# Kernel optimization log

Measured on AMD Instinct MI355X. Metric: run time of the kernel, lower is better.

The kernel has to match this reference:

```python
import jax, jax.numpy as jnp
import numpy as np

B, S, D, H = 64, 256, 1024, 1024
F0, F1 = 1024, 1024
STDV = 1.0 / np.sqrt(H)


def setup_inputs() -> dict:
    key = jax.random.key(0)
    ks = jax.random.split(key, 14)
    u = lambda k, shape: jax.random.uniform(k, shape, jnp.float32, -STDV, STDV)
    return {
        "input_feats": jax.random.normal(ks[0], (B, S, D), jnp.float32),
        "feat0": jax.random.normal(ks[1], (B, S, F0), jnp.float32),
        "feat1": jax.random.normal(ks[2], (B, S, F1), jnp.float32),
        "weight_ih": u(ks[3], (3 * H, D)),
        "weight_hh": u(ks[4], (3 * H, H)),
        "weight_fh0": u(ks[5], (2 * H, F0)),
        "weight_fh1": u(ks[6], (2 * H, F1)),
        "bias_ih": u(ks[7], (3 * H,)),
        "bias_hh": u(ks[8], (3 * H,)),
        "bias_fh0": u(ks[9], (2 * H,)),
        "bias_fh1": u(ks[10], (2 * H,)),
    }


def reference(input_feats, feat0, feat1, weight_ih, weight_hh, weight_fh0,
              weight_fh1, bias_ih, bias_hh, bias_fh0, bias_fh1):
    hid = weight_hh.shape[1]
    # Input-to-gate and feature-to-gate projections have no recurrence:
    # batch them over all timesteps up front (same math as per-step F.linear).
    gi = input_feats @ weight_ih.T + bias_ih                      # [B,S,3H]
    gf = (feat0 @ weight_fh0.T + feat1 @ weight_fh1.T
          + bias_fh0 + bias_fh1)                                  # [B,S,2H]
    gi_t = jnp.swapaxes(gi, 0, 1)                                 # [S,B,3H]
    gf_t = jnp.swapaxes(gf, 0, 1)                                 # [S,B,2H]

    def step(hx, xs):
        gi_s, gf_s = xs
        gh = hx @ weight_hh.T + bias_hh                           # [B,3H]
        i_r, i_i, i_n = jnp.split(gi_s, 3, axis=1)
        h_r, h_i, h_n = jnp.split(gh, 3, axis=1)
        f_r, f_i = jnp.split(gf_s, 2, axis=1)
        resetgate = jax.nn.sigmoid(i_r + h_r + f_r)
        inputgate = jax.nn.sigmoid(i_i + h_i + f_i)
        newgate = jnp.tanh(i_n + resetgate * h_n)
        hy = newgate + inputgate * (hx - newgate)
        return hy, hy

    h0 = jnp.zeros((input_feats.shape[0], hid), input_feats.dtype)
    h_last, ys = jax.lax.scan(step, h0, (gi_t, gf_t))
    output = jnp.swapaxes(ys, 0, 1)                               # [B,S,H]
    return output, h_last
```

## Files before the change

### kernel.cpp

```cpp
#include <hip/hip_runtime.h>

typedef unsigned short u16;
typedef __attribute__((ext_vector_type(8))) short short8;
typedef __attribute__((ext_vector_type(4))) float f32x4;
typedef __attribute__((ext_vector_type(4))) unsigned u32x4;

#define BB 64
#define SS 256
#define HH 1024
#define NG 3072
#define KK 1024
#define NOUT ((size_t)BB * SS * HH)

#define OFF_GSUM 0ull
#define OFF_HB0 100663296ull
#define OFF_HB1 100794368ull
#define OFF_BAR 100925440ull
#define WS_NEED 100925952ull

__device__ __forceinline__ float bf2f_u(unsigned x) {
  unsigned u = x << 16;
  float f;
  __builtin_memcpy(&f, &u, 4);
  return f;
}
__device__ __forceinline__ u16 f2bf(float f) {
  unsigned u;
  __builtin_memcpy(&u, &f, 4);
  u = (u + 0x7fffu + ((u >> 16) & 1u)) >> 16;
  return (u16)u;
}
__device__ __forceinline__ short8 cvt8(f32x4 lo, f32x4 hi) {
  union { unsigned u[4]; short8 s; } r;
  asm("v_cvt_pk_bf16_f32 %0, %1, %2" : "=v"(r.u[0]) : "v"(lo[0]), "v"(lo[1]));
  asm("v_cvt_pk_bf16_f32 %0, %1, %2" : "=v"(r.u[1]) : "v"(lo[2]), "v"(lo[3]));
  asm("v_cvt_pk_bf16_f32 %0, %1, %2" : "=v"(r.u[2]) : "v"(hi[0]), "v"(hi[1]));
  asm("v_cvt_pk_bf16_f32 %0, %1, %2" : "=v"(r.u[3]) : "v"(hi[2]), "v"(hi[3]));
  return r.s;
}
__device__ __forceinline__ float sigmoidf_(float x) {
  return __builtin_amdgcn_rcpf(1.f + __expf(-x));
}
__device__ __forceinline__ float tanhf_(float x) {
  return 2.f * __builtin_amdgcn_rcpf(1.f + __expf(-2.f * x)) - 1.f;
}

typedef const __attribute__((address_space(1))) void* gcptr;
typedef __attribute__((address_space(3))) void* lptr;

__global__ __launch_bounds__(256) void gemm_fused(
    const float* __restrict__ X, const float* __restrict__ F0, const float* __restrict__ F1,
    const float* __restrict__ Wih, const float* __restrict__ Wf0, const float* __restrict__ Wf1,
    const float* __restrict__ bih, const float* __restrict__ bf0, const float* __restrict__ bf1,
    u16* __restrict__ C) {
  __shared__ __align__(16) float ldsA[128 * 32];
  __shared__ __align__(16) float ldsB[128 * 32];
  const int t = threadIdx.x;
  const int nwg = gridDim.x;
  const int cpx = nwg >> 3;
  const int wg = (blockIdx.x & 7) * cpx + (blockIdx.x >> 3);
  const int ntn = NG / 128;
  const int m0 = (wg / ntn) * 128;
  const int n0 = (wg % ntn) * 128;
  const int lane = t & 63, wv = t >> 6;
  const int wm = wv >> 1, wn = wv & 1;

  f32x4 acc[4][4] = {};

  const int nsrc = (n0 < 2048) ? 3 : 1;
  for (int src = 0; src < nsrc; ++src) {
    const float* Ap = (src == 0) ? X : ((src == 1) ? F0 : F1);
    const float* Wp = (src == 0) ? Wih : ((src == 1) ? Wf0 : Wf1);
    const float* Abase = Ap + (size_t)m0 * KK;
    const float* Wbase = Wp + (size_t)n0 * KK;
    for (int k0 = 0; k0 < KK; k0 += 32) {
#pragma unroll
      for (int c = 0; c < 4; ++c) {
        const int idx = c * 256 + t;
        const int row = idx >> 3, q = idx & 7;
        const int qs = q ^ (row & 7);
        __builtin_amdgcn_global_load_lds((gcptr)(Abase + (size_t)row * KK + k0 + qs * 4),
                                         (lptr)(&ldsA[idx * 4]), 16, 0, 0);
        __builtin_amdgcn_global_load_lds((gcptr)(Wbase + (size_t)row * KK + k0 + qs * 4),
                                         (lptr)(&ldsB[idx * 4]), 16, 0, 0);
      }
      __syncthreads();
      short8 af[4], bw[4];
      const int g0 = (lane >> 4) * 2;
#pragma unroll
      for (int i = 0; i < 4; ++i) {
        {
          const int row = wm * 64 + i * 16 + (lane & 15);
          const int ga = g0 ^ (row & 7), gb = (g0 + 1) ^ (row & 7);
          f32x4 lo = *(const f32x4*)&ldsA[row * 32 + ga * 4];
          f32x4 hi = *(const f32x4*)&ldsA[row * 32 + gb * 4];
          af[i] = cvt8(lo, hi);
        }
        {
          const int row = wn * 64 + i * 16 + (lane & 15);
          const int ga = g0 ^ (row & 7), gb = (g0 + 1) ^ (row & 7);
          f32x4 lo = *(const f32x4*)&ldsB[row * 32 + ga * 4];
          f32x4 hi = *(const f32x4*)&ldsB[row * 32 + gb * 4];
          bw[i] = cvt8(lo, hi);
        }
      }
#pragma unroll
      for (int i = 0; i < 4; ++i)
#pragma unroll
        for (int j = 0; j < 4; ++j)
          acc[i][j] = __builtin_amdgcn_mfma_f32_16x16x32_bf16(af[i], bw[j], acc[i][j], 0, 0, 0);
      __syncthreads();
    }
  }
#pragma unroll
  for (int j = 0; j < 4; ++j) {
    const int col = n0 + wn * 64 + j * 16 + (lane & 15);
    float bias = bih[col];
    if (col < 2048) bias += bf0[col] + bf1[col];
#pragma unroll
    for (int i = 0; i < 4; ++i) {
      const int row = m0 + wm * 64 + i * 16 + (lane >> 4) * 4;
#pragma unroll
      for (int r = 0; r < 4; ++r)
        C[(size_t)(row + r) * NG + col] = f2bf(acc[i][j][r] + bias);
    }
  }
}

#define SB0() __builtin_amdgcn_sched_barrier(0)

#define ISSUE8(buf, bkk)                                                        \
  _Pragma("unroll")                                                             \
  for (int i_ = 0; i_ < 8; ++i_)                                                \
    asm volatile("global_load_dwordx4 %0, %1, off sc0 sc1"                      \
                 : "=&v"(buf[i_]) : "v"(ap + ((bkk) + i_) * 32));

#define CONSUME8(buf, bkk)                                                      \
  _Pragma("unroll")                                                             \
  for (int i_ = 0; i_ < 8; ++i_) {                                              \
    const int ko_ = ((bkk) + i_) * 64 + kb;                                     \
    short8 br_ = *(const short8*)(s0 + (ko_ ^ sw));                             \
    short8 bj_ = *(const short8*)(s1 + (ko_ ^ sw));                             \
    short8 bn_ = *(const short8*)(s2 + (ko_ ^ sw));                             \
    ar = __builtin_amdgcn_mfma_f32_16x16x32_bf16(buf[i_], br_, ar, 0, 0, 0);    \
    ai = __builtin_amdgcn_mfma_f32_16x16x32_bf16(buf[i_], bj_, ai, 0, 0, 0);    \
    an = __builtin_amdgcn_mfma_f32_16x16x32_bf16(buf[i_], bn_, an, 0, 0, 0);    \
  }

#define ISSUE_GSUM(snext)                                                       \
  _Pragma("unroll")                                                             \
  for (int r_ = 0; r_ < 4; ++r_) {                                              \
    const u16* gp_ = gsum + ((size_t)(mb + quad * 4 + r_) * 256 + (size_t)(snext)) * 3072 + jl; \
    asm volatile("global_load_ushort %0, %1, off" : "=&v"(pgu[r_ * 3 + 0]) : "v"(gp_));          \
    asm volatile("global_load_ushort %0, %1, off" : "=&v"(pgu[r_ * 3 + 1]) : "v"(gp_ + 1024));   \
    asm volatile("global_load_ushort %0, %1, off" : "=&v"(pgu[r_ * 3 + 2]) : "v"(gp_ + 2048));   \
  }

__global__ __launch_bounds__(256, 1) void scan_kernel(
    const u16* __restrict__ gsum, const float* __restrict__ Whh, const float* __restrict__ bhh,
    u16* __restrict__ h0buf, u16* __restrict__ h1buf,
    float* __restrict__ out, unsigned* __restrict__ bar) {
  extern __shared__ u16 wlds[];
  const int t = threadIdx.x, w = blockIdx.x;
  const int j0 = w * 16;
  for (int c = t; c < 48 * 128; c += 256) {
    int q = c >> 7, chunk = c & 127;
    int g = q >> 4, i = q & 15;
    const float* wf = Whh + ((size_t)(g * 1024 + j0 + i)) * 1024 + chunk * 8;
    short8 v = cvt8(*(const f32x4*)wf, *(const f32x4*)(wf + 4));
    *(short8*)((char*)wlds + q * 2048 + ((chunk * 16) ^ (i << 4))) = v;
  }
  const int lane = t & 63;
  const int bi = lane & 15;
  const int quad = lane >> 4;
  const int jl = j0 + bi;
  const int mb = (t >> 6) * 16;
  const float bhr = bhh[jl];
  const float bhi = bhh[1024 + jl];
  const float bhn = bhh[2048 + jl];
  __syncthreads();

  float hreg[4] = {0.f, 0.f, 0.f, 0.f};

  const int kb = quad * 16;
  const int sw = bi << 4;
  const char* wbytes = (const char*)wlds;
  const char* s0 = wbytes + (size_t)(0 + bi) * 2048;
  const char* s1 = wbytes + (size_t)(16 + bi) * 2048;
  const char* s2 = wbytes + (size_t)(32 + bi) * 2048;

  unsigned* myctr = bar + (w & 7);

  unsigned pgu[12];
  ISSUE_GSUM(0);
  asm volatile("s_waitcnt vmcnt(0)" ::: "memory");
  SB0();

  short8 aA[8], aB[8], aC[8], aD[8];
  for (int s = 0; s < 256; ++s) {
    f32x4 ar = {0.f, 0.f, 0.f, 0.f};
    f32x4 ai = {0.f, 0.f, 0.f, 0.f};
    f32x4 an = {0.f, 0.f, 0.f, 0.f};
    if (s > 0) {
      asm volatile("s_waitcnt vmcnt(24)" ::: "memory");
      SB0();
      CONSUME8(aA, 0);
      asm volatile("s_waitcnt vmcnt(16)" ::: "memory");
      SB0();
      CONSUME8(aB, 8);
      asm volatile("s_waitcnt vmcnt(8)" ::: "memory");
      SB0();
      CONSUME8(aC, 16);
      asm volatile("s_waitcnt vmcnt(0)" ::: "memory");
      SB0();
      CONSUME8(aD, 24);
      SB0();
    }
    u16* hw = (s & 1) ? h0buf : h1buf;
    float hy4[4];
    unsigned hv4[4];
#pragma unroll
    for (int r = 0; r < 4; ++r) {
      float rg = sigmoidf_(bf2f_u(pgu[r * 3 + 0]) + ar[r] + bhr);
      float ig = sigmoidf_(bf2f_u(pgu[r * 3 + 1]) + ai[r] + bhi);
      float ng = tanhf_(bf2f_u(pgu[r * 3 + 2]) + rg * (an[r] + bhn));
      float hy = ng + ig * (hreg[r] - ng);
      hreg[r] = hy;
      hy4[r] = hy;
      hv4[r] = (unsigned)f2bf(hy);
    }
    if (s < 255) {
#pragma unroll
      for (int r = 0; r < 4; ++r) {
        int b = mb + quad * 4 + r;
        asm volatile("global_store_short %0, %1, off sc0 sc1"
                     :: "v"(hw + (size_t)b * 1024 + jl), "v"(hv4[r]) : "memory");
      }
    }
#pragma unroll
    for (int r = 0; r < 4; ++r) {
      int b = mb + quad * 4 + r;
      size_t m = (size_t)b * 256 + s;
      asm volatile("global_store_dword %0, %1, off nt"
                   :: "v"(out + m * 1024 + jl), "v"(hy4[r]) : "memory");
    }
    if (s < 255) {
      ISSUE_GSUM(s + 1);
      asm volatile("s_waitcnt vmcnt(16)" ::: "memory");
      SB0();
      __builtin_amdgcn_s_barrier();
      if (t == 0) {
        unsigned one = 1;
        asm volatile("global_atomic_add %0, %1, off" :: "v"(myctr), "v"(one) : "memory");
      }
      if (lane == 0) {
        const unsigned target = 64u * (unsigned)(s + 1);
        for (;;) {
          u32x4 va, vb;
          asm volatile("global_load_dwordx4 %0, %2, off sc0 sc1\n\t"
                       "global_load_dwordx4 %1, %2, off offset:16 sc0 sc1\n\t"
                       "s_waitcnt vmcnt(0)"
                       : "=&v"(va), "=&v"(vb) : "v"(bar) : "memory");
          unsigned sum = va[0] + va[1] + va[2] + va[3] + vb[0] + vb[1] + vb[2] + vb[3];
          if (sum >= target) break;
          __builtin_amdgcn_s_sleep(1);
        }
      }
      SB0();
      const u16* ap = hw + (size_t)(mb + bi) * 1024 + quad * 8;
      ISSUE8(aA, 0);
      ISSUE8(aB, 8);
      ISSUE8(aC, 16);
      ISSUE8(aD, 24);
      SB0();
    }
  }
#pragma unroll
  for (int r = 0; r < 4; ++r) {
    int b = mb + quad * 4 + r;
    out[NOUT + (size_t)b * 1024 + jl] = hreg[r];
  }
}

extern "C" void kernel_launch(void* const* d_in, const int* in_sizes, int n_in,
                              void* d_out, int out_size, void* d_ws, size_t ws_size,
                              hipStream_t stream) {
  if (ws_size < WS_NEED) return;
  const float* x   = (const float*)d_in[0];
  const float* f0  = (const float*)d_in[1];
  const float* f1  = (const float*)d_in[2];
  const float* wih = (const float*)d_in[3];
  const float* whh = (const float*)d_in[4];
  const float* wf0 = (const float*)d_in[5];
  const float* wf1 = (const float*)d_in[6];
  const float* bih = (const float*)d_in[7];
  const float* bhh = (const float*)d_in[8];
  const float* bf0 = (const float*)d_in[9];
  const float* bf1 = (const float*)d_in[10];

  char* ws = (char*)d_ws;
  u16* gsum = (u16*)(ws + OFF_GSUM);
  u16* hb0 = (u16*)(ws + OFF_HB0);
  u16* hb1 = (u16*)(ws + OFF_HB1);
  unsigned* bar = (unsigned*)(ws + OFF_BAR);

  hipMemsetAsync(bar, 0, 128, stream);
  hipMemsetAsync(hb0, 0, 131072, stream);
  hipMemsetAsync(hb1, 0, 131072, stream);

  gemm_fused<<<dim3(3072), dim3(256), 0, stream>>>(x, f0, f1, wih, wf0, wf1, bih, bf0, bf1, gsum);

  hipFuncSetAttribute(reinterpret_cast<const void*>(&scan_kernel),
                      hipFuncAttributeMaxDynamicSharedMemorySize, 98304);
  scan_kernel<<<dim3(64), dim3(256), 98304, stream>>>(gsum, whh, bhh, hb0, hb1, (float*)d_out, bar);
}
```

Baseline: 2.613 ms.

## Add dedicated sync wavefront with staged per-quarter barrier relay through LDS

Adds a fifth wavefront per block that performs the grid-wide atomic arrive and polls the counters, publishing progress through an LDS relay variable. Counters are regrouped so each covers a contiguous group of 8 blocks, which lets the compute waves start loading each quarter of the hidden state as soon as the blocks producing it have arrived instead of waiting for all blocks. The goal is to overlap the cross-block barrier with the loads of h for the next step. The cost is an extra wave and LDS polling spins, plus timeout guards that could let a wave read stale data if a block is very late.

Result: slower. 4.458 ms (+70.6%).

```diff
diff --git a/kernel.cpp b/kernel.cpp
--- a/kernel.cpp
+++ b/kernel.cpp
@@ -156,14 +156,22 @@
     asm volatile("global_load_ushort %0, %1, off" : "=&v"(pgu[r_ * 3 + 2]) : "v"(gp_ + 2048));   \
   }
 
-__global__ __launch_bounds__(256, 1) void scan_kernel(
+#define POLL(K)                                                                 \
+  if (lane == 0) {                                                              \
+    int guard_ = 0;                                                             \
+    while (*(volatile int*)&relay < 4 * s + (K) + 1 && ++guard_ < (1 << 22)) {} \
+  }                                                                             \
+  SB0();
+
+__global__ __launch_bounds__(320, 1) void scan_kernel(
     const u16* __restrict__ gsum, const float* __restrict__ Whh, const float* __restrict__ bhh,
     u16* __restrict__ h0buf, u16* __restrict__ h1buf,
     float* __restrict__ out, unsigned* __restrict__ bar) {
   extern __shared__ u16 wlds[];
+  __shared__ int relay;
   const int t = threadIdx.x, w = blockIdx.x;
   const int j0 = w * 16;
-  for (int c = t; c < 48 * 128; c += 256) {
+  for (int c = t; c < 48 * 128; c += 320) {
     int q = c >> 7, chunk = c & 127;
     int g = q >> 4, i = q & 15;
     const float* wf = Whh + ((size_t)(g * 1024 + j0 + i)) * 1024 + chunk * 8;
@@ -171,16 +179,17 @@
     *(short8*)((char*)wlds + q * 2048 + ((chunk * 16) ^ (i << 4))) = v;
   }
   const int lane = t & 63;
+  const int wv = t >> 6;
   const int bi = lane & 15;
   const int quad = lane >> 4;
   const int jl = j0 + bi;
-  const int mb = (t >> 6) * 16;
+  const int mb = (wv & 3) * 16;
   const float bhr = bhh[jl];
   const float bhi = bhh[1024 + jl];
   const float bhn = bhh[2048 + jl];
+  unsigned* myctr = bar + (w >> 3);
+  if (t == 0) relay = 0;
   __syncthreads();
-
-  float hreg[4] = {0.f, 0.f, 0.f, 0.f};
 
   const int kb = quad * 16;
   const int sw = bi << 4;
@@ -189,8 +198,34 @@
   const char* s1 = wbytes + (size_t)(16 + bi) * 2048;
   const char* s2 = wbytes + (size_t)(32 + bi) * 2048;
 
-  unsigned* myctr = bar + (w & 7);
-
+  if (wv == 4) {
+    for (int s = 0; s < 255; ++s) {
+      __builtin_amdgcn_s_barrier();
+      if (lane == 0) {
+        unsigned one = 1;
+        asm volatile("global_atomic_add %0, %1, off" :: "v"(myctr), "v"(one) : "memory");
+        const unsigned tgt = 16u * (unsigned)(s + 1);
+        int lvl = 0, guard = 0;
+        while (lvl < 4) {
+          u32x4 va, vb;
+          asm volatile("global_load_dwordx4 %0, %2, off sc0 sc1\n\t"
+                       "global_load_dwordx4 %1, %2, off offset:16 sc0 sc1\n\t"
+                       "s_waitcnt vmcnt(0)"
+                       : "=&v"(va), "=&v"(vb) : "v"(bar) : "memory");
+          unsigned p0 = va[0] + va[1], p1 = va[2] + va[3];
+          unsigned p2 = vb[0] + vb[1], p3 = vb[2] + vb[3];
+          int nl = 0;
+          if (p0 >= tgt) { nl = 1; if (p1 >= tgt) { nl = 2; if (p2 >= tgt) { nl = 3; if (p3 >= tgt) nl = 4; } } }
+          if (nl > lvl) { lvl = nl; *(volatile int*)&relay = 4 * s + lvl; }
+          if (++guard > (1 << 18)) { *(volatile int*)&relay = 4 * s + 4; break; }
+          if (lvl < 4) __builtin_amdgcn_s_sleep(1);
+        }
+      }
+    }
+    return;
+  }
+
+  float hreg[4] = {0.f, 0.f, 0.f, 0.f};
   unsigned pgu[12];
   ISSUE_GSUM(0);
   asm volatile("s_waitcnt vmcnt(0)" ::: "memory");
@@ -249,28 +284,14 @@
       asm volatile("s_waitcnt vmcnt(16)" ::: "memory");
       SB0();
       __builtin_amdgcn_s_barrier();
-      if (t == 0) {
-        unsigned one = 1;
-        asm volatile("global_atomic_add %0, %1, off" :: "v"(myctr), "v"(one) : "memory");
-      }
-      if (lane == 0) {
-        const unsigned target = 64u * (unsigned)(s + 1);
-        for (;;) {
-          u32x4 va, vb;
-          asm volatile("global_load_dwordx4 %0, %2, off sc0 sc1\n\t"
-                       "global_load_dwordx4 %1, %2, off offset:16 sc0 sc1\n\t"
-                       "s_waitcnt vmcnt(0)"
-                       : "=&v"(va), "=&v"(vb) : "v"(bar) : "memory");
-          unsigned sum = va[0] + va[1] + va[2] + va[3] + vb[0] + vb[1] + vb[2] + vb[3];
-          if (sum >= target) break;
-          __builtin_amdgcn_s_sleep(1);
-        }
-      }
-      SB0();
       const u16* ap = hw + (size_t)(mb + bi) * 1024 + quad * 8;
+      POLL(0);
       ISSUE8(aA, 0);
+      POLL(1);
       ISSUE8(aB, 8);
+      POLL(2);
       ISSUE8(aC, 16);
+      POLL(3);
       ISSUE8(aD, 24);
       SB0();
     }
@@ -312,5 +333,5 @@
 
   hipFuncSetAttribute(reinterpret_cast<const void*>(&scan_kernel),
                       hipFuncAttributeMaxDynamicSharedMemorySize, 98304);
-  scan_kernel<<<dim3(64), dim3(256), 98304, stream>>>(gsum, whh, bhh, hb0, hb1, (float*)d_out, bar);
-}
+  scan_kernel<<<dim3(64), dim3(320), 98304, stream>>>(gsum, whh, bhh, hb0, hb1, (float*)d_out, bar);
+}
```
